# Optimization experiments

Measured on AMD Instinct MI355X. Metric: run time of the kernel, lower is better.

The kernel has to match this reference:

```python
import jax, jax.numpy as jnp
import numpy as np

N = 50000      # nodes
E = 800000     # edges (avg degree 16)
IN, H, OUT = 128, 256, 2
BN_EPS = 1e-5


def setup_inputs() -> dict:
    key = jax.random.key(0)
    ks = jax.random.split(key, 24)
    w = lambda k, s: jax.random.normal(k, s, jnp.float32) * 0.05
    inp = {
        "x": jax.random.normal(ks[0], (N, IN), jnp.float32),
        "edge_index": jax.random.randint(ks[1], (2, E), 0, N, jnp.int64),
    }
    # GINConv 1 MLP: Linear(IN,H) -> BN(H) -> ReLU -> Linear(H,H) -> ReLU
    inp.update(c1_W1=w(ks[2], (IN, H)), c1_b1=w(ks[3], (H,)),
               c1_g=jnp.ones((H,), jnp.float32), c1_be=jnp.zeros((H,), jnp.float32),
               c1_W2=w(ks[4], (H, H)), c1_b2=w(ks[5], (H,)))
    # GINConv 2
    inp.update(c2_W1=w(ks[6], (H, H)), c2_b1=w(ks[7], (H,)),
               c2_g=jnp.ones((H,), jnp.float32), c2_be=jnp.zeros((H,), jnp.float32),
               c2_W2=w(ks[8], (H, H)), c2_b2=w(ks[9], (H,)))
    # GINConv 3
    inp.update(c3_W1=w(ks[10], (H, H)), c3_b1=w(ks[11], (H,)),
               c3_g=jnp.ones((H,), jnp.float32), c3_be=jnp.zeros((H,), jnp.float32),
               c3_W2=w(ks[12], (H, H)), c3_b2=w(ks[13], (H,)))
    # readout head
    inp.update(lin1_W=w(ks[14], (3 * H, 3 * H)), lin1_b=w(ks[15], (3 * H,)),
               lin2_W=w(ks[16], (3 * H, OUT)), lin2_b=w(ks[17], (OUT,)))
    return inp


def _gin_conv(x, src, dst, W1, b1, g, be, W2, b2):
    # sum-aggregate neighbor features: agg[i] = sum_{e: dst[e]==i} x[src[e]]
    agg = jax.ops.segment_sum(x[src], dst, num_segments=N)
    h = (x + agg) @ W1 + b1            # (1+eps)*x + agg, eps=0
    mu = h.mean(axis=0)
    var = h.var(axis=0)                # biased var, as torch BN training
    h = jax.nn.relu((h - mu) * jax.lax.rsqrt(var + BN_EPS) * g + be)
    return jax.nn.relu(h @ W2 + b2)


def reference(x, edge_index,
              c1_W1, c1_b1, c1_g, c1_be, c1_W2, c1_b2,
              c2_W1, c2_b1, c2_g, c2_be, c2_W2, c2_b2,
              c3_W1, c3_b1, c3_g, c3_be, c3_W2, c3_b2,
              lin1_W, lin1_b, lin2_W, lin2_b):
    src, dst = edge_index[0], edge_index[1]
    h1 = _gin_conv(x, src, dst, c1_W1, c1_b1, c1_g, c1_be, c1_W2, c1_b2)
    h2 = _gin_conv(h1, src, dst, c2_W1, c2_b1, c2_g, c2_be, c2_W2, c2_b2)
    h3 = _gin_conv(h2, src, dst, c3_W1, c3_b1, c3_g, c3_be, c3_W2, c3_b2)
    h = jnp.concatenate((h1, h2, h3), axis=1)        # [N, 3H]
    h = jax.nn.relu(h @ lin1_W + lin1_b)
    h = h @ lin2_W + lin2_b                          # [N, OUT]
    return h, jax.nn.softmax(h, axis=1)
```

## Files before the change

kernel.cpp:

```cpp
#include <hip/hip_runtime.h>
#include <hip/hip_bf16.h>


#define GIN_N_FEAT_IN 128
#define GIN_H 256
#define M_PAD_ROWS 50048

typedef short short8 __attribute__((ext_vector_type(8)));
typedef float f32x4 __attribute__((ext_vector_type(4)));

__device__ inline ushort f32_to_bf16(float f) {
    union { float f; uint u; } x; x.f = f;
    uint r = x.u + 0x7fff + ((x.u >> 16) & 1);
    return (ushort)(r >> 16);
}
__device__ inline float bf16_to_f32(uint h) {
    union { uint u; float f; } x; x.u = h << 16;
    return x.f;
}
__device__ inline uint pack_bf16(float lo, float hi) {
    return (uint)f32_to_bf16(lo) | ((uint)f32_to_bf16(hi) << 16);
}

__device__ inline void gload_lds16(const ushort* g, ushort* l) {
    __builtin_amdgcn_global_load_lds(
        (const __attribute__((address_space(1))) void*)g,
        (__attribute__((address_space(3))) void*)l, 16, 0, 0);
}


__global__ void cvt_f32_bf16(const float* __restrict__ in, ushort* __restrict__ out, int npairs) {
    for (int i = blockIdx.x * blockDim.x + threadIdx.x; i < npairs; i += gridDim.x * blockDim.x) {
        float2 v = ((const float2*)in)[i];
        ((uint*)out)[i] = pack_bf16(v.x, v.y);
    }
}

__global__ void transpose_cvt(const float* __restrict__ in, ushort* __restrict__ out, int R, int C) {
    int idx = blockIdx.x * blockDim.x + threadIdx.x;
    if (idx >= R * C) return;
    int r = idx / C, c = idx - r * C;
    out[(size_t)c * R + r] = f32_to_bf16(in[idx]);
}


__global__ void count_kernel(const int* __restrict__ ei, int* __restrict__ deg, int E) {
    for (int e = blockIdx.x * blockDim.x + threadIdx.x; e < E; e += gridDim.x * blockDim.x) {
        atomicAdd(&deg[ei[E + e]], 1);
    }
}

__global__ void scan_chunk(const int* __restrict__ deg, int* __restrict__ row_start,
                           int* __restrict__ chunk_sums, int N) {
    __shared__ int sm[256];
    int tid = threadIdx.x;
    int idx = blockIdx.x * 256 + tid;
    int v = (idx < N) ? deg[idx] : 0;
    sm[tid] = v;
    __syncthreads();
    #pragma unroll
    for (int off = 1; off < 256; off <<= 1) {
        int t = (tid >= off) ? sm[tid - off] : 0;
        __syncthreads();
        sm[tid] += t;
        __syncthreads();
    }
    if (idx < N) row_start[idx] = sm[tid] - v;
    if (tid == 255) chunk_sums[blockIdx.x] = sm[255];
}

__global__ void scan_tops(int* __restrict__ chunk_sums, int* __restrict__ row_start,
                          int nchunks, int N, int E) {
    __shared__ int sm[256];
    int tid = threadIdx.x;
    int v = (tid < nchunks) ? chunk_sums[tid] : 0;
    sm[tid] = v;
    __syncthreads();
    #pragma unroll
    for (int off = 1; off < 256; off <<= 1) {
        int t = (tid >= off) ? sm[tid - off] : 0;
        __syncthreads();
        sm[tid] += t;
        __syncthreads();
    }
    if (tid < nchunks) chunk_sums[tid] = sm[tid] - v;
    if (tid == 0) row_start[N] = E;
}

__global__ void scan_add(int* __restrict__ row_start, int* __restrict__ cursor,
                         const int* __restrict__ chunk_sums, int N) {
    int idx = blockIdx.x * 256 + threadIdx.x;
    if (idx < N) {
        int v = row_start[idx] + chunk_sums[blockIdx.x];
        row_start[idx] = v;
        cursor[idx] = v;
    }
}

__global__ void scatter_kernel(const int* __restrict__ ei, int* __restrict__ cursor,
                               int* __restrict__ perm, int E) {
    for (int e = blockIdx.x * blockDim.x + threadIdx.x; e < E; e += gridDim.x * blockDim.x) {
        int d = ei[E + e];
        int pos = atomicAdd(&cursor[d], 1);
        perm[pos] = ei[e];
    }
}


template <int W>
__global__ void agg2(const ushort* __restrict__ xsrc, int stride,
                     const int* __restrict__ row_start, const int* __restrict__ perm,
                     ushort* __restrict__ out, int N) {
    constexpr int PL = W / 64;
    int node = blockIdx.x * 4 + (threadIdx.x >> 6);
    if (node >= N) return;
    const int lane = threadIdx.x & 63;
    const size_t loff = (size_t)lane * PL;

    float af[PL];
    {
        const ushort* p = xsrc + (size_t)node * stride + loff;
        if constexpr (W == 256) {
            uint2 v = *(const uint2*)p;
            af[0] = bf16_to_f32(v.x & 0xffffu); af[1] = bf16_to_f32(v.x >> 16);
            af[2] = bf16_to_f32(v.y & 0xffffu); af[3] = bf16_to_f32(v.y >> 16);
        } else {
            uint v = *(const uint*)p;
            af[0] = bf16_to_f32(v & 0xffffu); af[1] = bf16_to_f32(v >> 16);
        }
    }
    const int s = row_start[node], e = row_start[node + 1];
    int j = s;
    for (; j + 4 <= e; j += 4) {
        int n0 = perm[j], n1 = perm[j + 1], n2 = perm[j + 2], n3 = perm[j + 3];
        if constexpr (W == 256) {
            uint2 w0 = *(const uint2*)(xsrc + (size_t)n0 * stride + loff);
            uint2 w1 = *(const uint2*)(xsrc + (size_t)n1 * stride + loff);
            uint2 w2 = *(const uint2*)(xsrc + (size_t)n2 * stride + loff);
            uint2 w3 = *(const uint2*)(xsrc + (size_t)n3 * stride + loff);
            af[0] += bf16_to_f32(w0.x & 0xffffu) + bf16_to_f32(w1.x & 0xffffu)
                   + bf16_to_f32(w2.x & 0xffffu) + bf16_to_f32(w3.x & 0xffffu);
            af[1] += bf16_to_f32(w0.x >> 16) + bf16_to_f32(w1.x >> 16)
                   + bf16_to_f32(w2.x >> 16) + bf16_to_f32(w3.x >> 16);
            af[2] += bf16_to_f32(w0.y & 0xffffu) + bf16_to_f32(w1.y & 0xffffu)
                   + bf16_to_f32(w2.y & 0xffffu) + bf16_to_f32(w3.y & 0xffffu);
            af[3] += bf16_to_f32(w0.y >> 16) + bf16_to_f32(w1.y >> 16)
                   + bf16_to_f32(w2.y >> 16) + bf16_to_f32(w3.y >> 16);
        } else {
            uint w0 = *(const uint*)(xsrc + (size_t)n0 * stride + loff);
            uint w1 = *(const uint*)(xsrc + (size_t)n1 * stride + loff);
            uint w2 = *(const uint*)(xsrc + (size_t)n2 * stride + loff);
            uint w3 = *(const uint*)(xsrc + (size_t)n3 * stride + loff);
            af[0] += bf16_to_f32(w0 & 0xffffu) + bf16_to_f32(w1 & 0xffffu)
                   + bf16_to_f32(w2 & 0xffffu) + bf16_to_f32(w3 & 0xffffu);
            af[1] += bf16_to_f32(w0 >> 16) + bf16_to_f32(w1 >> 16)
                   + bf16_to_f32(w2 >> 16) + bf16_to_f32(w3 >> 16);
        }
    }
    for (; j < e; ++j) {
        int sn = perm[j];
        const ushort* p = xsrc + (size_t)sn * stride + loff;
        if constexpr (W == 256) {
            uint2 w = *(const uint2*)p;
            af[0] += bf16_to_f32(w.x & 0xffffu); af[1] += bf16_to_f32(w.x >> 16);
            af[2] += bf16_to_f32(w.y & 0xffffu); af[3] += bf16_to_f32(w.y >> 16);
        } else {
            uint w = *(const uint*)p;
            af[0] += bf16_to_f32(w & 0xffffu); af[1] += bf16_to_f32(w >> 16);
        }
    }
    ushort* po = out + (size_t)node * W + loff;
    if constexpr (W == 256) {
        uint2 o; o.x = pack_bf16(af[0], af[1]); o.y = pack_bf16(af[2], af[3]);
        *(uint2*)po = o;
    } else {
        *(uint*)po = pack_bf16(af[0], af[1]);
    }
}


template <int MODE>
__global__ __launch_bounds__(256) void gemm_mfma(
    const ushort* __restrict__ A, const ushort* __restrict__ Bt,
    const float* __restrict__ bias, void* __restrict__ Cout,
    int ldc, int K, const float* __restrict__ w2,
    float* __restrict__ extra, int Nvalid) {
    __shared__ ushort As[128 * 32];
    __shared__ ushort Bs[128 * 32];
    const int tid = threadIdx.x;

    const int gx = gridDim.x;
    const int nwg = gx * gridDim.y;
    const int flat = blockIdx.y * gx + blockIdx.x;
    const int q = nwg >> 3, r = nwg & 7;
    const int xcd = flat & 7, loc = flat >> 3;
    const int wg = (xcd < r ? xcd * (q + 1) : r * (q + 1) + (xcd - r) * q) + loc;
    const int bm = (wg / gx) * 128;
    const int bn = (wg % gx) * 128;

    const int lane = tid & 63;
    const int wid = tid >> 6;
    const int wr = wid >> 1, wc = wid & 1;

    f32x4 acc[4][4] = {};

    const int srow = tid >> 2;
    const int skcol = (tid & 3) * 8;
    const ushort* Ag0 = A + (size_t)(bm + srow) * K + skcol;
    const ushort* Ag1 = A + (size_t)(bm + 64 + srow) * K + skcol;
    const ushort* Bg0 = Bt + (size_t)(bn + srow) * K + skcol;
    const ushort* Bg1 = Bt + (size_t)(bn + 64 + srow) * K + skcol;
    ushort* As0 = &As[(tid & ~63) * 8];
    ushort* As1 = &As[2048 + (tid & ~63) * 8];
    ushort* Bs0 = &Bs[(tid & ~63) * 8];
    ushort* Bs1 = &Bs[2048 + (tid & ~63) * 8];

    const int kk = (lane >> 4) * 8;
    const int fr = lane & 15;

    for (int k0 = 0; k0 < K; k0 += 32) {
        gload_lds16(Ag0 + k0, As0);
        gload_lds16(Ag1 + k0, As1);
        gload_lds16(Bg0 + k0, Bs0);
        gload_lds16(Bg1 + k0, Bs1);
        __syncthreads();
        short8 af[4], bf[4];
        #pragma unroll
        for (int m = 0; m < 4; ++m)
            af[m] = *(const short8*)&As[(wr * 64 + m * 16 + fr) * 32 + kk];
        #pragma unroll
        for (int n = 0; n < 4; ++n)
            bf[n] = *(const short8*)&Bs[(wc * 64 + n * 16 + fr) * 32 + kk];
        #pragma unroll
        for (int m = 0; m < 4; ++m)
            #pragma unroll
            for (int n = 0; n < 4; ++n)
                acc[m][n] = __builtin_amdgcn_mfma_f32_16x16x32_bf16(af[m], bf[n], acc[m][n], 0, 0, 0);
        __syncthreads();
    }

    if constexpr (MODE == 2) {
        #pragma unroll
        for (int m = 0; m < 4; ++m) {
            #pragma unroll
            for (int rr = 0; rr < 4; ++rr) {
                float o0 = 0.f, o1 = 0.f;
                #pragma unroll
                for (int n = 0; n < 4; ++n) {
                    int col = bn + wc * 64 + n * 16 + fr;
                    float v = fmaxf(acc[m][n][rr] + bias[col], 0.f);
                    o0 = fmaf(v, w2[col * 2 + 0], o0);
                    o1 = fmaf(v, w2[col * 2 + 1], o1);
                }
                o0 += __shfl_xor(o0, 1); o1 += __shfl_xor(o1, 1);
                o0 += __shfl_xor(o0, 2); o1 += __shfl_xor(o1, 2);
                o0 += __shfl_xor(o0, 4); o1 += __shfl_xor(o1, 4);
                o0 += __shfl_xor(o0, 8); o1 += __shfl_xor(o1, 8);
                int row = bm + wr * 64 + m * 16 + (lane >> 4) * 4 + rr;
                if (fr == 0 && row < Nvalid) {
                    atomicAdd(&extra[(size_t)row * 2 + 0], o0);
                    atomicAdd(&extra[(size_t)row * 2 + 1], o1);
                }
            }
        }
    } else {
        float s1[4], s2[4];
        if constexpr (MODE == 0) {
            #pragma unroll
            for (int n = 0; n < 4; ++n) { s1[n] = 0.f; s2[n] = 0.f; }
        }
        #pragma unroll
        for (int n = 0; n < 4; ++n) {
            const int col = bn + wc * 64 + n * 16 + fr;
            const float bv = bias[col];
            #pragma unroll
            for (int m = 0; m < 4; ++m) {
                const int row0 = bm + wr * 64 + m * 16 + (lane >> 4) * 4;
                #pragma unroll
                for (int rr = 0; rr < 4; ++rr) {
                    float v = acc[m][n][rr] + bv;
                    if constexpr (MODE == 1) {
                        v = fmaxf(v, 0.f);
                        ((ushort*)Cout)[(size_t)(row0 + rr) * ldc + col] = f32_to_bf16(v);
                    } else {
                        ((float*)Cout)[(size_t)(row0 + rr) * ldc + col] = v;
                        if (row0 + rr < Nvalid) { s1[n] += v; s2[n] += v * v; }
                    }
                }
            }
        }
        if constexpr (MODE == 0) {
            #pragma unroll
            for (int n = 0; n < 4; ++n) {
                float a = s1[n], b = s2[n];
                a += __shfl_xor(a, 16); b += __shfl_xor(b, 16);
                a += __shfl_xor(a, 32); b += __shfl_xor(b, 32);
                if ((lane >> 4) == 0) {
                    int col = bn + wc * 64 + n * 16 + fr;
                    atomicAdd(&extra[col], a);
                    atomicAdd(&extra[256 + col], b);
                }
            }
        }
    }
}


__global__ void bn_apply(const float* __restrict__ h, const float* __restrict__ sums,
                         const float* __restrict__ g, const float* __restrict__ be,
                         ushort* __restrict__ outb, int Nrows) {
    int total = Nrows * 128;
    float inv = 1.0f / (float)Nrows;
    for (int idx = blockIdx.x * blockDim.x + threadIdx.x; idx < total;
         idx += gridDim.x * blockDim.x) {
        int row = idx >> 7;
        int cp = (idx & 127) * 2;
        float2 v = *(const float2*)(h + (size_t)row * 256 + cp);
        float mu0 = sums[cp] * inv,     mu1 = sums[cp + 1] * inv;
        float va0 = sums[256 + cp] * inv - mu0 * mu0;
        float va1 = sums[257 + cp] * inv - mu1 * mu1;
        float o0 = fmaxf((v.x - mu0) * rsqrtf(va0 + 1e-5f) * g[cp]     + be[cp],     0.f);
        float o1 = fmaxf((v.y - mu1) * rsqrtf(va1 + 1e-5f) * g[cp + 1] + be[cp + 1], 0.f);
        *(uint*)(outb + (size_t)row * 256 + cp) = pack_bf16(o0, o1);
    }
}


__global__ void finalize(const float* __restrict__ acc, const float* __restrict__ b2,
                         float* __restrict__ out, int Nrows) {
    int i = blockIdx.x * blockDim.x + threadIdx.x;
    if (i >= Nrows) return;
    float h0 = acc[2 * i] + b2[0];
    float h1 = acc[2 * i + 1] + b2[1];
    out[2 * i] = h0;
    out[2 * i + 1] = h1;
    float m = fmaxf(h0, h1);
    float e0 = expf(h0 - m), e1 = expf(h1 - m);
    float s = e0 + e1;
    out[(size_t)2 * Nrows + 2 * i] = e0 / s;
    out[(size_t)2 * Nrows + 2 * i + 1] = e1 / s;
}


extern "C" void kernel_launch(void* const* d_in, const int* in_sizes, int n_in,
                              void* d_out, int out_size, void* d_ws, size_t ws_size,
                              hipStream_t stream) {
    const int N = in_sizes[0] / GIN_N_FEAT_IN;
    const int E = in_sizes[1] / 2;
    const int MP = M_PAD_ROWS;
    const int nchunks = (N + 255) / 256;

    const float* x  = (const float*)d_in[0];
    const int*   ei = (const int*)d_in[1];
    const float* cW1[3] = {(const float*)d_in[2],  (const float*)d_in[8],  (const float*)d_in[14]};
    const float* cb1[3] = {(const float*)d_in[3],  (const float*)d_in[9],  (const float*)d_in[15]};
    const float* cg [3] = {(const float*)d_in[4],  (const float*)d_in[10], (const float*)d_in[16]};
    const float* cbe[3] = {(const float*)d_in[5],  (const float*)d_in[11], (const float*)d_in[17]};
    const float* cW2[3] = {(const float*)d_in[6],  (const float*)d_in[12], (const float*)d_in[18]};
    const float* cb2[3] = {(const float*)d_in[7],  (const float*)d_in[13], (const float*)d_in[19]};
    const float* lin1_W = (const float*)d_in[20];
    const float* lin1_b = (const float*)d_in[21];
    const float* lin2_W = (const float*)d_in[22];
    const float* lin2_b = (const float*)d_in[23];
    float* out = (float*)d_out;

    char* ws = (char*)d_ws;
    size_t off = 0;
    auto carve = [&](size_t bytes) {
        void* p = ws + off;
        off += (bytes + 255) & ~(size_t)255;
        return p;
    };
    ushort* Hcat   = (ushort*)carve((size_t)MP * 768 * 2);
    float*  hlin   = (float*) carve((size_t)MP * 256 * 4);
    ushort* hlin_b = (ushort*)carve((size_t)MP * 256 * 2);
    ushort* hpre   = (ushort*)carve((size_t)MP * 256 * 2);
    ushort* xb     = (ushort*)carve((size_t)MP * 128 * 2);
    ushort* w1t[3] = {(ushort*)carve(256 * 256 * 2), (ushort*)carve(256 * 256 * 2),
                      (ushort*)carve(256 * 256 * 2)};
    ushort* w2t[3] = {(ushort*)carve(256 * 256 * 2), (ushort*)carve(256 * 256 * 2),
                      (ushort*)carve(256 * 256 * 2)};
    ushort* lin1t  = (ushort*)carve((size_t)768 * 768 * 2);
    int*   row_st  = (int*)carve((size_t)(N + 1) * 4);
    int*   cursor  = (int*)carve((size_t)N * 4);
    int*   perm    = (int*)carve((size_t)E * 4);
    int*   csums   = (int*)carve(256 * 4);
    float* bnsums  = (float*)carve(512 * 4);
    float* out_acc = (float*)carve((size_t)N * 2 * 4);
    (void)ws_size;

    cvt_f32_bf16<<<1024, 256, 0, stream>>>(x, xb, N * 64);
    transpose_cvt<<<(128 * 256 + 255) / 256, 256, 0, stream>>>(cW1[0], w1t[0], 128, 256);
    transpose_cvt<<<(256 * 256 + 255) / 256, 256, 0, stream>>>(cW1[1], w1t[1], 256, 256);
    transpose_cvt<<<(256 * 256 + 255) / 256, 256, 0, stream>>>(cW1[2], w1t[2], 256, 256);
    for (int L = 0; L < 3; ++L)
        transpose_cvt<<<(256 * 256 + 255) / 256, 256, 0, stream>>>(cW2[L], w2t[L], 256, 256);
    transpose_cvt<<<(768 * 768 + 255) / 256, 256, 0, stream>>>(lin1_W, lin1t, 768, 768);

    hipMemsetAsync(cursor, 0, (size_t)N * 4, stream);
    count_kernel<<<1024, 256, 0, stream>>>(ei, cursor, E);
    scan_chunk<<<nchunks, 256, 0, stream>>>(cursor, row_st, csums, N);
    scan_tops<<<1, 256, 0, stream>>>(csums, row_st, nchunks, N, E);
    scan_add<<<nchunks, 256, 0, stream>>>(row_st, cursor, csums, N);
    scatter_kernel<<<1024, 256, 0, stream>>>(ei, cursor, perm, E);

    const dim3 ggrid(2, MP / 128);
    const int aggblocks = (N + 3) / 4;

    for (int L = 0; L < 3; ++L) {
        if (L == 0)
            agg2<128><<<aggblocks, 256, 0, stream>>>(xb, 128, row_st, perm, hpre, N);
        else
            agg2<256><<<aggblocks, 256, 0, stream>>>(Hcat + (size_t)(L - 1) * 256, 768,
                                                     row_st, perm, hpre, N);

        hipMemsetAsync(bnsums, 0, 512 * 4, stream);
        gemm_mfma<0><<<ggrid, 256, 0, stream>>>(
            hpre, w1t[L], cb1[L], hlin, 256, (L == 0) ? 128 : 256,
            nullptr, bnsums, N);

        bn_apply<<<2048, 256, 0, stream>>>(hlin, bnsums, cg[L], cbe[L], hlin_b, N);

        gemm_mfma<1><<<ggrid, 256, 0, stream>>>(
            hlin_b, w2t[L], cb2[L], (void*)(Hcat + (size_t)L * 256), 768, 256,
            nullptr, nullptr, 0);
    }

    hipMemsetAsync(out_acc, 0, (size_t)N * 2 * 4, stream);
    gemm_mfma<2><<<dim3(6, MP / 128), 256, 0, stream>>>(
        Hcat, lin1t, lin1_b, nullptr, 0, 768, lin2_W, out_acc, N);

    finalize<<<(N + 255) / 256, 256, 0, stream>>>(out_acc, lin2_b, out, N);
}
```

Before: 725.3 us.

## Add dedicated head GEMM with larger tiles and per-tile partials, batch weight prep

Replaces the generic MODE 2 head GEMM with a 512-thread kernel using 256x128 tiles and K-step 64, which reduces per-iteration barriers and increases reuse. Lin2 partial sums are reduced in shared memory and written per column tile to a partial buffer, replacing global atomics and the output memset. The final kernel then sums the six partials. The seven weight transpose launches are merged into one batched launch. Row padding grows to a multiple of 256, which adds a little padded work and LDS use per block.

```diff
diff --git a/kernel.cpp b/kernel.cpp
--- a/kernel.cpp
+++ b/kernel.cpp
@@ -4,7 +4,7 @@
 
 #define GIN_N_FEAT_IN 128
 #define GIN_H 256
-#define M_PAD_ROWS 50048
+#define M_PAD_ROWS 50176
 
 typedef short short8 __attribute__((ext_vector_type(8)));
 typedef float f32x4 __attribute__((ext_vector_type(4)));
@@ -36,11 +36,24 @@
     }
 }
 
-__global__ void transpose_cvt(const float* __restrict__ in, ushort* __restrict__ out, int R, int C) {
-    int idx = blockIdx.x * blockDim.x + threadIdx.x;
-    if (idx >= R * C) return;
-    int r = idx / C, c = idx - r * C;
-    out[(size_t)c * R + r] = f32_to_bf16(in[idx]);
+struct WPrep {
+    const float* src[7];
+    ushort* dst[7];
+    int R[7];
+    int C[7];
+};
+
+__global__ void prep_weights(WPrep p) {
+    int which = blockIdx.y;
+    int R = p.R[which], C = p.C[which];
+    int total = R * C;
+    const float* src = p.src[which];
+    ushort* dst = p.dst[which];
+    for (int idx = blockIdx.x * blockDim.x + threadIdx.x; idx < total;
+         idx += gridDim.x * blockDim.x) {
+        int r = idx / C, c = idx - r * C;
+        dst[(size_t)c * R + r] = f32_to_bf16(src[idx]);
+    }
 }
 
 
@@ -183,8 +196,7 @@
 __global__ __launch_bounds__(256) void gemm_mfma(
     const ushort* __restrict__ A, const ushort* __restrict__ Bt,
     const float* __restrict__ bias, void* __restrict__ Cout,
-    int ldc, int K, const float* __restrict__ w2,
-    float* __restrict__ extra, int Nvalid) {
+    int ldc, int K, float* __restrict__ extra, int Nvalid) {
     __shared__ ushort As[128 * 32];
     __shared__ ushort Bs[128 * 32];
     const int tid = threadIdx.x;
@@ -239,69 +251,139 @@
         __syncthreads();
     }
 
-    if constexpr (MODE == 2) {
+    float s1[4], s2[4];
+    if constexpr (MODE == 0) {
+        #pragma unroll
+        for (int n = 0; n < 4; ++n) { s1[n] = 0.f; s2[n] = 0.f; }
+    }
+    #pragma unroll
+    for (int n = 0; n < 4; ++n) {
+        const int col = bn + wc * 64 + n * 16 + fr;
+        const float bv = bias[col];
         #pragma unroll
         for (int m = 0; m < 4; ++m) {
+            const int row0 = bm + wr * 64 + m * 16 + (lane >> 4) * 4;
             #pragma unroll
             for (int rr = 0; rr < 4; ++rr) {
-                float o0 = 0.f, o1 = 0.f;
-                #pragma unroll
-                for (int n = 0; n < 4; ++n) {
-                    int col = bn + wc * 64 + n * 16 + fr;
-                    float v = fmaxf(acc[m][n][rr] + bias[col], 0.f);
-                    o0 = fmaf(v, w2[col * 2 + 0], o0);
-                    o1 = fmaf(v, w2[col * 2 + 1], o1);
-                }
-                o0 += __shfl_xor(o0, 1); o1 += __shfl_xor(o1, 1);
-                o0 += __shfl_xor(o0, 2); o1 += __shfl_xor(o1, 2);
-                o0 += __shfl_xor(o0, 4); o1 += __shfl_xor(o1, 4);
-                o0 += __shfl_xor(o0, 8); o1 += __shfl_xor(o1, 8);
-                int row = bm + wr * 64 + m * 16 + (lane >> 4) * 4 + rr;
-                if (fr == 0 && row < Nvalid) {
-                    atomicAdd(&extra[(size_t)row * 2 + 0], o0);
-                    atomicAdd(&extra[(size_t)row * 2 + 1], o1);
+                float v = acc[m][n][rr] + bv;
+                if constexpr (MODE == 1) {
+                    v = fmaxf(v, 0.f);
+                    ((ushort*)Cout)[(size_t)(row0 + rr) * ldc + col] = f32_to_bf16(v);
+                } else {
+                    ((float*)Cout)[(size_t)(row0 + rr) * ldc + col] = v;
+                    if (row0 + rr < Nvalid) { s1[n] += v; s2[n] += v * v; }
                 }
             }
         }
-    } else {
-        float s1[4], s2[4];
-        if constexpr (MODE == 0) {
+    }
+    if constexpr (MODE == 0) {
+        #pragma unroll
+        for (int n = 0; n < 4; ++n) {
+            float a = s1[n], b = s2[n];
+            a += __shfl_xor(a, 16); b += __shfl_xor(b, 16);
+            a += __shfl_xor(a, 32); b += __shfl_xor(b, 32);
+            if ((lane >> 4) == 0) {
+                int col = bn + wc * 64 + n * 16 + fr;
+                atomicAdd(&extra[col], a);
+                atomicAdd(&extra[256 + col], b);
+            }
+        }
+    }
+}
+
+
+__global__ __launch_bounds__(512) void gemm_head(
+    const ushort* __restrict__ A,
+    const ushort* __restrict__ Bt,
+    const float* __restrict__ bias,
+    const float* __restrict__ w2,
+    float* __restrict__ part,
+    int K, int MP) {
+    __shared__ ushort As[256 * 64];
+    __shared__ ushort Bs[128 * 64];
+    __shared__ float sm_part[256][2];
+    const int tid = threadIdx.x;
+
+    const int gx = gridDim.x;
+    const int nwg = gx * gridDim.y;
+    const int flat = blockIdx.y * gx + blockIdx.x;
+    const int q = nwg >> 3, r = nwg & 7;
+    const int xcd = flat & 7, loc = flat >> 3;
+    const int wg = (xcd < r ? xcd * (q + 1) : r * (q + 1) + (xcd - r) * q) + loc;
+    const int bm = (wg / gx) * 256;
+    const int bn = (wg % gx) * 128;
+    const int coltile = wg % gx;
+
+    const int lane = tid & 63;
+    const int wid = tid >> 6;
+    const int wr = wid >> 1;
+    const int wc = wid & 1;
+
+    sm_part[tid >> 1][tid & 1] = 0.f;
+
+    f32x4 acc[4][4] = {};
+
+    const int grow = tid >> 3;
+    const int gcol = (tid & 7) * 8;
+    const int wbase = (tid & ~63) * 8;
+    const int kko = (lane >> 4) * 8;
+    const int fr = lane & 15;
+
+    for (int k0 = 0; k0 < K; k0 += 64) {
+        #pragma unroll
+        for (int c = 0; c < 4; ++c)
+            gload_lds16(A + (size_t)(bm + c * 64 + grow) * K + k0 + gcol,
+                        &As[c * 4096 + wbase]);
+        #pragma unroll
+        for (int c = 0; c < 2; ++c)
+            gload_lds16(Bt + (size_t)(bn + c * 64 + grow) * K + k0 + gcol,
+                        &Bs[c * 4096 + wbase]);
+        __syncthreads();
+        #pragma unroll
+        for (int ksub = 0; ksub < 2; ++ksub) {
+            short8 af[4], bf[4];
             #pragma unroll
-            for (int n = 0; n < 4; ++n) { s1[n] = 0.f; s2[n] = 0.f; }
-        }
-        #pragma unroll
-        for (int n = 0; n < 4; ++n) {
-            const int col = bn + wc * 64 + n * 16 + fr;
-            const float bv = bias[col];
+            for (int m = 0; m < 4; ++m)
+                af[m] = *(const short8*)&As[(wr * 64 + m * 16 + fr) * 64 + ksub * 32 + kko];
             #pragma unroll
-            for (int m = 0; m < 4; ++m) {
-                const int row0 = bm + wr * 64 + m * 16 + (lane >> 4) * 4;
+            for (int n = 0; n < 4; ++n)
+                bf[n] = *(const short8*)&Bs[(wc * 64 + n * 16 + fr) * 64 + ksub * 32 + kko];
+            #pragma unroll
+            for (int m = 0; m < 4; ++m)
                 #pragma unroll
-                for (int rr = 0; rr < 4; ++rr) {
-                    float v = acc[m][n][rr] + bv;
-                    if constexpr (MODE == 1) {
-                        v = fmaxf(v, 0.f);
-                        ((ushort*)Cout)[(size_t)(row0 + rr) * ldc + col] = f32_to_bf16(v);
-                    } else {
-                        ((float*)Cout)[(size_t)(row0 + rr) * ldc + col] = v;
-                        if (row0 + rr < Nvalid) { s1[n] += v; s2[n] += v * v; }
-                    }
-                }
-            }
-        }
-        if constexpr (MODE == 0) {
+                for (int n = 0; n < 4; ++n)
+                    acc[m][n] = __builtin_amdgcn_mfma_f32_16x16x32_bf16(af[m], bf[n], acc[m][n], 0, 0, 0);
+        }
+        __syncthreads();
+    }
+
+    #pragma unroll
+    for (int m = 0; m < 4; ++m) {
+        #pragma unroll
+        for (int rr = 0; rr < 4; ++rr) {
+            float o0 = 0.f, o1 = 0.f;
             #pragma unroll
             for (int n = 0; n < 4; ++n) {
-                float a = s1[n], b = s2[n];
-                a += __shfl_xor(a, 16); b += __shfl_xor(b, 16);
-                a += __shfl_xor(a, 32); b += __shfl_xor(b, 32);
-                if ((lane >> 4) == 0) {
-                    int col = bn + wc * 64 + n * 16 + fr;
-                    atomicAdd(&extra[col], a);
-                    atomicAdd(&extra[256 + col], b);
-                }
+                int col = bn + wc * 64 + n * 16 + fr;
+                float v = fmaxf(acc[m][n][rr] + bias[col], 0.f);
+                o0 = fmaf(v, w2[col * 2 + 0], o0);
+                o1 = fmaf(v, w2[col * 2 + 1], o1);
             }
-        }
+            o0 += __shfl_xor(o0, 1); o1 += __shfl_xor(o1, 1);
+            o0 += __shfl_xor(o0, 2); o1 += __shfl_xor(o1, 2);
+            o0 += __shfl_xor(o0, 4); o1 += __shfl_xor(o1, 4);
+            o0 += __shfl_xor(o0, 8); o1 += __shfl_xor(o1, 8);
+            if (fr == 0) {
+                int lrow = wr * 64 + m * 16 + (lane >> 4) * 4 + rr;
+                atomicAdd(&sm_part[lrow][0], o0);
+                atomicAdd(&sm_part[lrow][1], o1);
+            }
+        }
+    }
+    __syncthreads();
+    {
+        int lrow = tid >> 1, comp = tid & 1;
+        part[((size_t)coltile * MP + bm + lrow) * 2 + comp] = sm_part[lrow][comp];
     }
 }
 
@@ -326,12 +408,16 @@
 }
 
 
-__global__ void finalize(const float* __restrict__ acc, const float* __restrict__ b2,
-                         float* __restrict__ out, int Nrows) {
+__global__ void finalize6(const float* __restrict__ part, const float* __restrict__ b2,
+                          float* __restrict__ out, int Nrows, int MP) {
     int i = blockIdx.x * blockDim.x + threadIdx.x;
     if (i >= Nrows) return;
-    float h0 = acc[2 * i] + b2[0];
-    float h1 = acc[2 * i + 1] + b2[1];
+    float h0 = b2[0], h1 = b2[1];
+    #pragma unroll
+    for (int c = 0; c < 6; ++c) {
+        h0 += part[((size_t)c * MP + i) * 2 + 0];
+        h1 += part[((size_t)c * MP + i) * 2 + 1];
+    }
     out[2 * i] = h0;
     out[2 * i + 1] = h1;
     float m = fmaxf(h0, h1);
@@ -386,16 +472,19 @@
     int*   perm    = (int*)carve((size_t)E * 4);
     int*   csums   = (int*)carve(256 * 4);
     float* bnsums  = (float*)carve(512 * 4);
-    float* out_acc = (float*)carve((size_t)N * 2 * 4);
+    float* part    = (float*)carve((size_t)6 * MP * 2 * 4);
     (void)ws_size;
 
     cvt_f32_bf16<<<1024, 256, 0, stream>>>(x, xb, N * 64);
-    transpose_cvt<<<(128 * 256 + 255) / 256, 256, 0, stream>>>(cW1[0], w1t[0], 128, 256);
-    transpose_cvt<<<(256 * 256 + 255) / 256, 256, 0, stream>>>(cW1[1], w1t[1], 256, 256);
-    transpose_cvt<<<(256 * 256 + 255) / 256, 256, 0, stream>>>(cW1[2], w1t[2], 256, 256);
-    for (int L = 0; L < 3; ++L)
-        transpose_cvt<<<(256 * 256 + 255) / 256, 256, 0, stream>>>(cW2[L], w2t[L], 256, 256);
-    transpose_cvt<<<(768 * 768 + 255) / 256, 256, 0, stream>>>(lin1_W, lin1t, 768, 768);
+    WPrep wp;
+    wp.src[0] = cW1[0]; wp.dst[0] = w1t[0]; wp.R[0] = 128; wp.C[0] = 256;
+    wp.src[1] = cW1[1]; wp.dst[1] = w1t[1]; wp.R[1] = 256; wp.C[1] = 256;
+    wp.src[2] = cW1[2]; wp.dst[2] = w1t[2]; wp.R[2] = 256; wp.C[2] = 256;
+    wp.src[3] = cW2[0]; wp.dst[3] = w2t[0]; wp.R[3] = 256; wp.C[3] = 256;
+    wp.src[4] = cW2[1]; wp.dst[4] = w2t[1]; wp.R[4] = 256; wp.C[4] = 256;
+    wp.src[5] = cW2[2]; wp.dst[5] = w2t[2]; wp.R[5] = 256; wp.C[5] = 256;
+    wp.src[6] = lin1_W; wp.dst[6] = lin1t;  wp.R[6] = 768; wp.C[6] = 768;
+    prep_weights<<<dim3(576, 7), 256, 0, stream>>>(wp);
 
     hipMemsetAsync(cursor, 0, (size_t)N * 4, stream);
     count_kernel<<<1024, 256, 0, stream>>>(ei, cursor, E);
@@ -416,19 +505,17 @@
 
         hipMemsetAsync(bnsums, 0, 512 * 4, stream);
         gemm_mfma<0><<<ggrid, 256, 0, stream>>>(
-            hpre, w1t[L], cb1[L], hlin, 256, (L == 0) ? 128 : 256,
-            nullptr, bnsums, N);
+            hpre, w1t[L], cb1[L], hlin, 256, (L == 0) ? 128 : 256, bnsums, N);
 
         bn_apply<<<2048, 256, 0, stream>>>(hlin, bnsums, cg[L], cbe[L], hlin_b, N);
 
         gemm_mfma<1><<<ggrid, 256, 0, stream>>>(
             hlin_b, w2t[L], cb2[L], (void*)(Hcat + (size_t)L * 256), 768, 256,
-            nullptr, nullptr, 0);
-    }
-
-    hipMemsetAsync(out_acc, 0, (size_t)N * 2 * 4, stream);
-    gemm_mfma<2><<<dim3(6, MP / 128), 256, 0, stream>>>(
-        Hcat, lin1t, lin1_b, nullptr, 0, 768, lin2_W, out_acc, N);
-
-    finalize<<<(N + 255) / 256, 256, 0, stream>>>(out_acc, lin2_b, out, N);
-}
+            nullptr, 0);
+    }
+
+    gemm_head<<<dim3(6, MP / 256), 512, 0, stream>>>(
+        Hcat, lin1t, lin1_b, lin2_W, part, 768, MP);
+
+    finalize6<<<(N + 255) / 256, 256, 0, stream>>>(part, lin2_b, out, N, MP);
+}
```

After: 686.9 us. 5.3% less time.
